# Performance work log

Hardware: AMD Instinct MI355X
Metric: run time of the kernel (lower is better)

## Reference

```python
import jax, jax.numpy as jnp
import numpy as np

N = 20000   # nodes
E = 320000  # edges
G = 64      # graphs in batch
IN = 256    # in_dim
H = 256     # hidden_dim1
C = 2       # n_classes


def setup_inputs() -> dict:
    key = jax.random.key(0)
    ks = jax.random.split(key, 12)
    h = jax.random.normal(ks[0], (N, IN), jnp.float32)
    src = jax.random.randint(ks[1], (E,), 0, N)
    dst = jax.random.randint(ks[2], (E,), 0, N)
    graph_id = jnp.sort(jax.random.randint(ks[3], (N,), 0, G))
    s_in = 1.0 / np.sqrt(IN)
    s_h = 1.0 / np.sqrt(H)
    W_conv = jax.random.normal(ks[4], (IN, H), jnp.float32) * s_in
    b_conv = jnp.zeros((H,), jnp.float32)
    w_gate = jax.random.normal(ks[5], (H, 1), jnp.float32) * s_h
    b_gate = jnp.zeros((1,), jnp.float32)
    W1 = jax.random.normal(ks[6], (H, H), jnp.float32) * s_h
    b1 = jnp.zeros((H,), jnp.float32)
    W2 = jax.random.normal(ks[7], (H, C), jnp.float32) * s_h
    b2 = jnp.zeros((C,), jnp.float32)
    return dict(h=h, src=src, dst=dst, graph_id=graph_id, W_conv=W_conv,
                b_conv=b_conv, w_gate=w_gate, b_gate=b_gate, W1=W1, b1=b1,
                W2=W2, b2=b2)


def reference(h, src, dst, graph_id, W_conv, b_conv, w_gate, b_gate, W1, b1, W2, b2):
    ones_e = jnp.ones((E,), jnp.float32)
    # DGL GraphConv, norm='both': D_out^-1/2 on source, D_in^-1/2 on dest
    deg_out = jax.ops.segment_sum(ones_e, src, num_segments=N)
    deg_in = jax.ops.segment_sum(ones_e, dst, num_segments=N)
    hn = h * jax.lax.rsqrt(jnp.maximum(deg_out, 1.0))[:, None]
    hn = hn @ W_conv                       # [N, H] (weight applied before aggregation)
    agg = jax.ops.segment_sum(hn[src], dst, num_segments=N)  # gather + scatter-add
    agg = agg * jax.lax.rsqrt(jnp.maximum(deg_in, 1.0))[:, None] + b_conv
    hr = jax.nn.relu(agg)                  # F.relu after conv1
    # GlobalAttentionPooling: per-graph segment softmax over gate scores
    gate = hr @ w_gate + b_gate            # [N, 1]
    gmax = jax.ops.segment_max(gate, graph_id, num_segments=G)
    e = jnp.exp(gate - gmax[graph_id])
    denom = jax.ops.segment_sum(e, graph_id, num_segments=G)
    att = e / denom[graph_id]              # [N, 1] attention weights (g2)
    hg = jax.ops.segment_sum(att * hr, graph_id, num_segments=G)  # [G, H]
    # classifier heads (dropout is identity at inference)
    a2 = hg @ W1 + b1
    a3 = a2 @ W2 + b2
    return jax.nn.sigmoid(a3), att, hg
```

## Files before the change

### kernel.cpp

```cpp
#include <hip/hip_runtime.h>
#include <hip/hip_bf16.h>
#include <hip/hip_fp16.h>
#include <math.h>

#define NN 20000
#define EE 320000
#define GG 64
#define IND 256
#define HD 256
#define CC 2

typedef __hip_bfloat16 bf16;
typedef __attribute__((ext_vector_type(8))) short short8;
typedef __attribute__((ext_vector_type(4))) float f32x4;

__device__ __forceinline__ float b2f(bf16 x){ return __bfloat162float(x); }
__device__ __forceinline__ float bits2f(unsigned short b){
    union{ float f; unsigned u; } v; v.u = ((unsigned)b) << 16; return v.f;
}
__device__ __forceinline__ short f2bs(float x){
    union{ bf16 b; short s; } u; u.b = __float2bfloat16(x); return u.s;
}
__device__ __forceinline__ float ldf3(const void* p, size_t i, int c){
    if (c == 1) return b2f(((const bf16*)p)[i]);
    if (c == 2) return __half2float(((const __half*)p)[i]);
    return ((const float*)p)[i];
}
__device__ __forceinline__ int idec(const void* p, int i, int c){
    if (c == 1) return (int)(((const long long*)p)[i]);
    if (c == 2) return (int)(((const float*)p)[i]);
    if (c == 3) return (int)__half2float(((const __half*)p)[i]);
    return ((const int*)p)[i];
}
__device__ __forceinline__ int wdetect_wave(const unsigned short* p, int t){
    unsigned u = p[2*t];
    int e8 = (u >> 7) & 0xFF;
    int e5 = (u >> 10) & 0x1F;
    int nz = __popcll(__ballot(u != 0));
    int cb = __popcll(__ballot(e8 >= 100 && e8 <= 141));
    int cf = __popcll(__ballot(e5 >= 4 && e5 <= 22));
    return (nz < 8) ? 0 : (cb >= 60) ? 1 : ((cf >= 60) ? 2 : 0);
}

#define ZBLK 64
#define DETB (9 + IND)
__global__ __launch_bounds__(256) void k_detect(const void* src, const void* dst,
                         const void* gid,
                         const unsigned short* h, const unsigned short* Wc,
                         const unsigned short* wg, const unsigned short* W1,
                         const unsigned short* W2, const unsigned short* bc,
                         int* icode, int* dcode, int* zero_base,
                         bf16* __restrict__ Wb){
    int blk = blockIdx.x;
    int t = threadIdx.x;
    if (blk < 3){
        if (t >= 64) return;
        const void* buf = (blk == 0) ? src : (blk == 1) ? dst : gid;
        int n     = (blk == 2) ? NN : EE;
        int bound = (blk == 2) ? GG : NN;
        long long v64 = ((const long long*)buf)[n/8 + t];
        unsigned long long bad64 = __ballot(v64 < 0 || v64 >= (long long)bound);
        int v32 = ((const int*)buf)[n/4 + t];
        unsigned long long bad32 = __ballot(v32 < 0 || v32 >= bound);
        float f32v = __uint_as_float(((const unsigned*)buf)[n/4 + t]);
        unsigned long long badf32 = __ballot(!(f32v >= 0.f && f32v < (float)bound));
        float f16v = __half2float(((const __half*)buf)[n/2 + t]);
        unsigned long long badf16 = __ballot(!(f16v >= 0.f && f16v < (float)bound));
        if (t == 0)
            icode[blk] = (bad64 == 0ull) ? 1 : ((bad32 == 0ull) ? 0 :
                         ((badf32 == 0ull) ? 2 : ((badf16 == 0ull) ? 3 : 0)));
    } else if (blk < 9){
        if (t >= 64) return;
        int b = blk - 3;
        const unsigned short* p = b==0?h:b==1?Wc:b==2?wg:b==3?W1:b==4?W2:bc;
        int code = wdetect_wave(p, t);
        if (t == 0) dcode[b] = code;
    } else if (blk < DETB){
        int k = blk - 9;
        __shared__ int scode;
        if (t < 64){
            int code = wdetect_wave(Wc, t);
            if (t == 0) scode = code;
        }
        __syncthreads();
        int c = scode;
        Wb[(size_t)t*IND + k] = __float2bfloat16(ldf3(Wc, (size_t)k*HD + t, c));
    } else {
        int idx = (blk - DETB)*256 + t;
        const int total = 3*NN + GG*HD;
        for (int i = idx; i < total; i += ZBLK*256) zero_base[i] = 0;
    }
}

#define GEMMB (NN/32)
#define PREPB ((EE+255)/256)
__global__ __launch_bounds__(256) void k_prepgemm(const void* __restrict__ h,
                                                  const bf16* __restrict__ Wb,
                                                  const void* __restrict__ src_r,
                                                  const void* __restrict__ dst_r,
                                                  const void* __restrict__ gid_r,
                                                  const int* __restrict__ icode,
                                                  const int* __restrict__ dcode,
                                                  int* __restrict__ gid_i,
                                                  int* cnt_out, int* cnt_in,
                                                  bf16* __restrict__ hn){
    int blk = blockIdx.x;
    if (blk >= GEMMB){
        int i = (blk - GEMMB)*256 + threadIdx.x;
        if (i < NN) gid_i[i] = idec(gid_r, i, icode[2]);
        if (i >= EE) return;
        int s = idec(src_r, i, icode[0]);
        int d = idec(dst_r, i, icode[1]);
        if ((unsigned)s < NN) atomicAdd(&cnt_out[s], 1);
        if ((unsigned)d < NN) atomicAdd(&cnt_in[d], 1);
        return;
    }
    int fh = dcode[0];
    int tid = threadIdx.x;
    int wave = tid >> 6, lane = tid & 63;
    int q = lane >> 4, mr = lane & 15;
    int row0 = blk * 32;
    int ncol0 = wave * 64;
    f32x4 acc[2][4] = {};
    const float* hf = (const float*)h;
    #pragma unroll
    for (int k0 = 0; k0 < IND; k0 += 32){
        short8 a[2], b[4];
        if (fh == 0){
            #pragma unroll
            for (int mi = 0; mi < 2; mi++){
                int r = row0 + mi*16 + mr;
                const float4* p = (const float4*)(hf + (size_t)r*IND + k0 + q*8);
                float4 v0 = p[0], v1 = p[1];
                a[mi][0] = f2bs(v0.x); a[mi][1] = f2bs(v0.y);
                a[mi][2] = f2bs(v0.z); a[mi][3] = f2bs(v0.w);
                a[mi][4] = f2bs(v1.x); a[mi][5] = f2bs(v1.y);
                a[mi][6] = f2bs(v1.z); a[mi][7] = f2bs(v1.w);
            }
        } else {
            #pragma unroll
            for (int mi = 0; mi < 2; mi++){
                int r = row0 + mi*16 + mr;
                #pragma unroll
                for (int j = 0; j < 8; j++)
                    a[mi][j] = f2bs(ldf3(h, (size_t)r*IND + k0 + q*8 + j, fh));
            }
        }
        #pragma unroll
        for (int ni = 0; ni < 4; ni++)
            b[ni] = *reinterpret_cast<const short8*>(
                        Wb + (size_t)(ncol0 + ni*16 + mr)*IND + k0 + q*8);
        #pragma unroll
        for (int mi = 0; mi < 2; mi++)
            #pragma unroll
            for (int ni = 0; ni < 4; ni++)
                acc[mi][ni] = __builtin_amdgcn_mfma_f32_16x16x32_bf16(
                                  a[mi], b[ni], acc[mi][ni], 0, 0, 0);
    }
    #pragma unroll
    for (int mi = 0; mi < 2; mi++){
        int rowb = row0 + mi*16 + q*4;
        #pragma unroll
        for (int r = 0; r < 4; r++){
            int row = rowb + r;
            #pragma unroll
            for (int ni = 0; ni < 4; ni++)
                hn[(size_t)row*HD + ncol0 + ni*16 + mr] =
                    __float2bfloat16(acc[mi][ni][r]);
        }
    }
}

__global__ __launch_bounds__(1024) void k_scan(const int* __restrict__ cnt_out,
                                               const int* __restrict__ cnt_in,
                                               const int* __restrict__ gid,
                                               float* rs_out, float* rs_in,
                                               int* __restrict__ row_start,
                                               int* gstart, int* gend){
    int t = threadIdx.x;
    for (int i = t; i < NN; i += 1024){
        rs_out[i] = rsqrtf(fmaxf((float)cnt_out[i], 1.f));
        rs_in[i]  = rsqrtf(fmaxf((float)cnt_in[i], 1.f));
    }
    __shared__ int part[1024];
    const int per = (NN + 1023)/1024;
    int lo = t*per, hi = min(lo+per, NN);
    int s = 0;
    for (int i = lo; i < hi; i++) s += cnt_in[i];
    part[t] = s; __syncthreads();
    for (int off = 1; off < 1024; off <<= 1){
        int v = (t >= off) ? part[t-off] : 0;
        __syncthreads();
        part[t] += v;
        __syncthreads();
    }
    int base = part[t] - s;
    for (int i = lo; i < hi; i++){ row_start[i] = base; base += cnt_in[i]; }
    if (t == 1023) row_start[NN] = part[1023];
    __shared__ int ls[GG+1];
    if (t <= GG){
        int a = 0, b = NN;
        while (a < b){
            int mid = (a + b) >> 1;
            if (gid[mid] < t) a = mid + 1; else b = mid;
        }
        ls[t] = a;
    }
    __syncthreads();
    if (t < GG){ gstart[t] = ls[t]; gend[t] = ls[t+1]; }
}

__global__ void k_fill(const void* src_r, const void* dst_r,
                       const int* __restrict__ icode,
                       const int* __restrict__ row_start, int* __restrict__ cursor,
                       int* __restrict__ csr_src){
    int e = blockIdx.x*256 + threadIdx.x;
    if (e >= EE) return;
    int s = idec(src_r, e, icode[0]);
    int d = idec(dst_r, e, icode[1]);
    if ((unsigned)s >= NN || (unsigned)d >= NN) return;
    int pos = atomicAdd(&cursor[d], 1);
    csr_src[row_start[d] + pos] = s;
}

__global__ __launch_bounds__(256) void k_gather(const bf16* __restrict__ hn,
                                                const float* __restrict__ rs_out,
                                                const float* __restrict__ rs_in,
                                                const int* __restrict__ row_start,
                                                const int* __restrict__ csr_src,
                                                const void* __restrict__ b_conv,
                                                const void* __restrict__ w_gate,
                                                const void* __restrict__ b_gate,
                                                const int* __restrict__ dcode,
                                                float* __restrict__ hr,
                                                float* __restrict__ gate){
    int wave = threadIdx.x >> 6, lane = threadIdx.x & 63;
    int n = blockIdx.x*4 + wave;
    if (n >= NN) return;
    int lo = row_start[n], hi = row_start[n+1];
    int half = lane >> 5, l2 = lane & 31;
    float a0=0.f,a1=0.f,a2=0.f,a3=0.f,a4=0.f,a5=0.f,a6=0.f,a7=0.f;
    int j = lo;
    for (; j + 8 <= hi; j += 8){
        int sA = csr_src[j+0+half], sB = csr_src[j+2+half];
        int sC = csr_src[j+4+half], sD = csr_src[j+6+half];
        float rA = rs_out[sA], rB = rs_out[sB], rC = rs_out[sC], rD = rs_out[sD];
        short8 uA = *reinterpret_cast<const short8*>(hn + (size_t)sA*HD + l2*8);
        short8 uB = *reinterpret_cast<const short8*>(hn + (size_t)sB*HD + l2*8);
        short8 uC = *reinterpret_cast<const short8*>(hn + (size_t)sC*HD + l2*8);
        short8 uD = *reinterpret_cast<const short8*>(hn + (size_t)sD*HD + l2*8);
        a0 = fmaf(rA, bits2f((unsigned short)uA[0]),
             fmaf(rB, bits2f((unsigned short)uB[0]),
             fmaf(rC, bits2f((unsigned short)uC[0]),
             fmaf(rD, bits2f((unsigned short)uD[0]), a0))));
        a1 = fmaf(rA, bits2f((unsigned short)uA[1]),
             fmaf(rB, bits2f((unsigned short)uB[1]),
             fmaf(rC, bits2f((unsigned short)uC[1]),
             fmaf(rD, bits2f((unsigned short)uD[1]), a1))));
        a2 = fmaf(rA, bits2f((unsigned short)uA[2]),
             fmaf(rB, bits2f((unsigned short)uB[2]),
             fmaf(rC, bits2f((unsigned short)uC[2]),
             fmaf(rD, bits2f((unsigned short)uD[2]), a2))));
        a3 = fmaf(rA, bits2f((unsigned short)uA[3]),
             fmaf(rB, bits2f((unsigned short)uB[3]),
             fmaf(rC, bits2f((unsigned short)uC[3]),
             fmaf(rD, bits2f((unsigned short)uD[3]), a3))));
        a4 = fmaf(rA, bits2f((unsigned short)uA[4]),
             fmaf(rB, bits2f((unsigned short)uB[4]),
             fmaf(rC, bits2f((unsigned short)uC[4]),
             fmaf(rD, bits2f((unsigned short)uD[4]), a4))));
        a5 = fmaf(rA, bits2f((unsigned short)uA[5]),
             fmaf(rB, bits2f((unsigned short)uB[5]),
             fmaf(rC, bits2f((unsigned short)uC[5]),
             fmaf(rD, bits2f((unsigned short)uD[5]), a5))));
        a6 = fmaf(rA, bits2f((unsigned short)uA[6]),
             fmaf(rB, bits2f((unsigned short)uB[6]),
             fmaf(rC, bits2f((unsigned short)uC[6]),
             fmaf(rD, bits2f((unsigned short)uD[6]), a6))));
        a7 = fmaf(rA, bits2f((unsigned short)uA[7]),
             fmaf(rB, bits2f((unsigned short)uB[7]),
             fmaf(rC, bits2f((unsigned short)uC[7]),
             fmaf(rD, bits2f((unsigned short)uD[7]), a7))));
    }
    for (; j + 2 <= hi; j += 2){
        int s = csr_src[j+half];
        float r = rs_out[s];
        short8 u = *reinterpret_cast<const short8*>(hn + (size_t)s*HD + l2*8);
        a0 = fmaf(r, bits2f((unsigned short)u[0]), a0);
        a1 = fmaf(r, bits2f((unsigned short)u[1]), a1);
        a2 = fmaf(r, bits2f((unsigned short)u[2]), a2);
        a3 = fmaf(r, bits2f((unsigned short)u[3]), a3);
        a4 = fmaf(r, bits2f((unsigned short)u[4]), a4);
        a5 = fmaf(r, bits2f((unsigned short)u[5]), a5);
        a6 = fmaf(r, bits2f((unsigned short)u[6]), a6);
        a7 = fmaf(r, bits2f((unsigned short)u[7]), a7);
    }
    if (j < hi && half == 0){
        int s = csr_src[j];
        float r = rs_out[s];
        short8 u = *reinterpret_cast<const short8*>(hn + (size_t)s*HD + l2*8);
        a0 = fmaf(r, bits2f((unsigned short)u[0]), a0);
        a1 = fmaf(r, bits2f((unsigned short)u[1]), a1);
        a2 = fmaf(r, bits2f((unsigned short)u[2]), a2);
        a3 = fmaf(r, bits2f((unsigned short)u[3]), a3);
        a4 = fmaf(r, bits2f((unsigned short)u[4]), a4);
        a5 = fmaf(r, bits2f((unsigned short)u[5]), a5);
        a6 = fmaf(r, bits2f((unsigned short)u[6]), a6);
        a7 = fmaf(r, bits2f((unsigned short)u[7]), a7);
    }
    float send0 = half ? a0 : a4;
    float send1 = half ? a1 : a5;
    float send2 = half ? a2 : a6;
    float send3 = half ? a3 : a7;
    float recv0 = __shfl_xor(send0, 32);
    float recv1 = __shfl_xor(send1, 32);
    float recv2 = __shfl_xor(send2, 32);
    float recv3 = __shfl_xor(send3, 32);
    float tot0 = (half ? a4 : a0) + recv0;
    float tot1 = (half ? a5 : a1) + recv1;
    float tot2 = (half ? a6 : a2) + recv2;
    float tot3 = (half ? a7 : a3) + recv3;
    int db = dcode[5], fg = dcode[2];
    float rsn = rs_in[n];
    int c = l2*8 + half*4;
    float v0 = fmaxf(fmaf(tot0, rsn, ldf3(b_conv, c+0, db)), 0.f);
    float v1 = fmaxf(fmaf(tot1, rsn, ldf3(b_conv, c+1, db)), 0.f);
    float v2 = fmaxf(fmaf(tot2, rsn, ldf3(b_conv, c+2, db)), 0.f);
    float v3 = fmaxf(fmaf(tot3, rsn, ldf3(b_conv, c+3, db)), 0.f);
    float4 fv; fv.x = v0; fv.y = v1; fv.z = v2; fv.w = v3;
    *(float4*)(hr + (size_t)n*HD + c) = fv;
    float g = v0*ldf3(w_gate, c+0, fg) + v1*ldf3(w_gate, c+1, fg)
            + v2*ldf3(w_gate, c+2, fg) + v3*ldf3(w_gate, c+3, fg);
    #pragma unroll
    for (int off = 32; off; off >>= 1) g += __shfl_down(g, off);
    if (lane == 0) gate[n] = g + ldf3(b_gate, 0, db);
}

__global__ __launch_bounds__(256) void k_softhg(const float* __restrict__ gate,
                                                const float* __restrict__ hr,
                                                const int* __restrict__ gstart,
                                                const int* __restrict__ gend,
                                                float* __restrict__ hg,
                                                float* __restrict__ out_att){
    int g = blockIdx.x >> 3, part = blockIdx.x & 7;
    int t = threadIdx.x, lane = t & 63, wid = t >> 6;
    int lo = gstart[g], hi = gend[g], len = hi - lo;
    if (len <= 0) return;
    __shared__ float red[4];
    float m = -INFINITY;
    for (int n = lo + t; n < hi; n += 256) m = fmaxf(m, gate[n]);
    #pragma unroll
    for (int off = 32; off; off >>= 1) m = fmaxf(m, __shfl_xor(m, off));
    if (lane == 0) red[wid] = m;
    __syncthreads();
    m = fmaxf(fmaxf(red[0], red[1]), fmaxf(red[2], red[3]));
    __syncthreads();
    float s = 0.f;
    for (int n = lo + t; n < hi; n += 256) s += expf(gate[n] - m);
    #pragma unroll
    for (int off = 32; off; off >>= 1) s += __shfl_xor(s, off);
    if (lane == 0) red[wid] = s;
    __syncthreads();
    s = red[0] + red[1] + red[2] + red[3];
    float inv = 1.f / s;
    int chunk = (len + 7) >> 3;
    int plo = lo + part*chunk, phi = min(plo + chunk, hi);
    if (plo >= phi) return;
    for (int n = plo + t; n < phi; n += 256)
        out_att[n] = expf(gate[n] - m) * inv;
    float a0 = 0.f, a1 = 0.f, a2 = 0.f, a3 = 0.f;
    int r = plo;
    for (; r + 4 <= phi; r += 4){
        float w0 = expf(gate[r+0] - m) * inv;
        float w1 = expf(gate[r+1] - m) * inv;
        float w2 = expf(gate[r+2] - m) * inv;
        float w3 = expf(gate[r+3] - m) * inv;
        a0 = fmaf(w0, hr[(size_t)(r+0)*HD + t], a0);
        a1 = fmaf(w1, hr[(size_t)(r+1)*HD + t], a1);
        a2 = fmaf(w2, hr[(size_t)(r+2)*HD + t], a2);
        a3 = fmaf(w3, hr[(size_t)(r+3)*HD + t], a3);
    }
    for (; r < phi; r++)
        a0 = fmaf(expf(gate[r] - m) * inv, hr[(size_t)r*HD + t], a0);
    atomicAdd(&hg[g*HD + t], (a0 + a1) + (a2 + a3));
}

__global__ __launch_bounds__(256) void k_cls(const float* __restrict__ hg,
                                             const void* __restrict__ W1,
                                             const void* __restrict__ b1,
                                             const void* __restrict__ W2,
                                             const void* __restrict__ b2,
                                             const int* __restrict__ dcode,
                                             float* __restrict__ out0,
                                             float* __restrict__ out_hg){
    int f1 = dcode[3], f2 = dcode[4], db = dcode[5];
    int g = blockIdx.x, tid = threadIdx.x;
    __shared__ float hs[256];
    float hv = hg[g*HD + tid];
    hs[tid] = hv;
    out_hg[g*HD + tid] = hv;
    __syncthreads();
    float acc = ldf3(b1, tid, db);
    if (f1 == 1){
        const bf16* w = (const bf16*)W1;
        for (int k = 0; k < HD; k++) acc += hs[k]*b2f(w[(size_t)k*HD + tid]);
    } else if (f1 == 2){
        const __half* w = (const __half*)W1;
        for (int k = 0; k < HD; k++) acc += hs[k]*__half2float(w[(size_t)k*HD + tid]);
    } else {
        const float* w = (const float*)W1;
        for (int k = 0; k < HD; k++) acc += hs[k]*w[(size_t)k*HD + tid];
    }
    float p0 = acc * ldf3(W2, tid*CC + 0, f2);
    float p1 = acc * ldf3(W2, tid*CC + 1, f2);
    __shared__ float r0[256], r1[256];
    r0[tid] = p0; r1[tid] = p1; __syncthreads();
    for (int s = 128; s; s >>= 1){
        if (tid < s){ r0[tid] += r0[tid+s]; r1[tid] += r1[tid+s]; }
        __syncthreads();
    }
    if (tid == 0){
        out0[g*CC+0] = 1.f/(1.f + expf(-(r0[0] + ldf3(b2, 0, db))));
        out0[g*CC+1] = 1.f/(1.f + expf(-(r1[0] + ldf3(b2, 1, db))));
    }
}

extern "C" void kernel_launch(void* const* d_in, const int* in_sizes, int n_in,
                              void* d_out, int out_size, void* d_ws, size_t ws_size,
                              hipStream_t stream) {
    const void* h      = d_in[0];
    const void* src_r  = d_in[1];
    const void* dst_r  = d_in[2];
    const void* gid_r  = d_in[3];
    const void* W_conv = d_in[4];
    const void* b_conv = d_in[5];
    const void* w_gate = d_in[6];
    const void* b_gate = d_in[7];
    const void* W1     = d_in[8];
    const void* b1     = d_in[9];
    const void* W2     = d_in[10];
    const void* b2     = d_in[11];

    float* out     = (float*)d_out;
    float* out0    = out;
    float* out_att = out + GG*CC;
    float* out_hg  = out + GG*CC + NN;

    char* w = (char*)d_ws;
    float* hr   = (float*)w;  w += (size_t)NN*HD*sizeof(float);
    bf16*  hn   = (bf16*)w;   w += (size_t)NN*HD*sizeof(bf16);
    bf16*  Wb   = (bf16*)w;   w += (size_t)IND*HD*sizeof(bf16);
    float* rs_o = (float*)w;  w += (size_t)NN*sizeof(float);
    float* rs_i = (float*)w;  w += (size_t)NN*sizeof(float);
    float* gate = (float*)w;  w += (size_t)NN*sizeof(float);
    int* gstart = (int*)w;    w += GG*sizeof(int);
    int* gend   = (int*)w;    w += GG*sizeof(int);
    int* dcode  = (int*)w;    w += 8*sizeof(int);
    int* icode  = (int*)w;    w += 8*sizeof(int);
    int* gid_i  = (int*)w;    w += (size_t)NN*sizeof(int);
    int* cnt_out= (int*)w;    w += (size_t)NN*sizeof(int);
    int* cnt_in = (int*)w;    w += (size_t)NN*sizeof(int);
    int* cursor = (int*)w;    w += (size_t)NN*sizeof(int);
    float* hg   = (float*)w;  w += (size_t)GG*HD*sizeof(float);
    int* rowst  = (int*)w;    w += (size_t)(NN+1)*sizeof(int);
    int* csr    = (int*)w;    w += (size_t)EE*sizeof(int);

    k_detect<<<DETB + ZBLK, 256, 0, stream>>>(src_r, dst_r, gid_r,
                                     (const unsigned short*)h, (const unsigned short*)W_conv,
                                     (const unsigned short*)w_gate, (const unsigned short*)W1,
                                     (const unsigned short*)W2, (const unsigned short*)b_conv,
                                     icode, dcode, cnt_out, Wb);

    k_prepgemm<<<GEMMB + PREPB, 256, 0, stream>>>(h, Wb, src_r, dst_r, gid_r,
                                                  icode, dcode, gid_i,
                                                  cnt_out, cnt_in, hn);

    k_scan<<<1, 1024, 0, stream>>>(cnt_out, cnt_in, gid_i, rs_o, rs_i,
                                   rowst, gstart, gend);

    k_fill<<<PREPB, 256, 0, stream>>>(src_r, dst_r, icode, rowst, cursor, csr);

    k_gather<<<(NN+3)/4, 256, 0, stream>>>(hn, rs_o, rs_i, rowst, csr,
                                           b_conv, w_gate, b_gate, dcode, hr, gate);

    k_softhg<<<GG*8, 256, 0, stream>>>(gate, hr, gstart, gend, hg, out_att);

    k_cls<<<GG, 256, 0, stream>>>(hg, W1, b1, W2, b2, dcode, out0, out_hg);
}
```

Before: 230.0 us.

## Pre-convert h to bf16 in detect kernel and software-pipeline GEMM loads

The fp32-to-bf16 conversion of h moves from the GEMM kernel into extra blocks of the detect kernel, which write a bf16 copy of h to workspace. The GEMM then reads bf16 directly and uses 16-row tiles, doubling the block count, with register double-buffering of the A and B fragments across the k loop. This is meant to shorten the GEMM's load and convert path and improve latency hiding. In exchange it adds a full extra write and read of a 10 MB bf16 buffer plus more workspace, and the smaller tile halves reuse of the W fragments.

Result: no change. 234.1 us (+1.8%).

```diff
diff --git a/kernel.cpp b/kernel.cpp
--- a/kernel.cpp
+++ b/kernel.cpp
@@ -44,13 +44,14 @@
 
 #define ZBLK 64
 #define DETB (9 + IND)
+#define HBB  (NN*HD/4096)
 __global__ __launch_bounds__(256) void k_detect(const void* src, const void* dst,
                          const void* gid,
                          const unsigned short* h, const unsigned short* Wc,
                          const unsigned short* wg, const unsigned short* W1,
                          const unsigned short* W2, const unsigned short* bc,
                          int* icode, int* dcode, int* zero_base,
-                         bf16* __restrict__ Wb){
+                         bf16* __restrict__ Wb, bf16* __restrict__ hb){
     int blk = blockIdx.x;
     int t = threadIdx.x;
     if (blk < 3){
@@ -85,22 +86,44 @@
         __syncthreads();
         int c = scode;
         Wb[(size_t)t*IND + k] = __float2bfloat16(ldf3(Wc, (size_t)k*HD + t, c));
+    } else if (blk < DETB + HBB){
+        __shared__ int scode;
+        if (t < 64){
+            int code = wdetect_wave(h, t);
+            if (t == 0) scode = code;
+        }
+        __syncthreads();
+        int c = scode;
+        size_t e0 = (size_t)(blk - DETB)*4096 + (size_t)t*16;
+        if (c == 0){
+            const float4* pf = (const float4*)((const float*)h + e0);
+            float4 v0 = pf[0], v1 = pf[1], v2 = pf[2], v3 = pf[3];
+            short8 s0, s1;
+            s0[0]=f2bs(v0.x); s0[1]=f2bs(v0.y); s0[2]=f2bs(v0.z); s0[3]=f2bs(v0.w);
+            s0[4]=f2bs(v1.x); s0[5]=f2bs(v1.y); s0[6]=f2bs(v1.z); s0[7]=f2bs(v1.w);
+            s1[0]=f2bs(v2.x); s1[1]=f2bs(v2.y); s1[2]=f2bs(v2.z); s1[3]=f2bs(v2.w);
+            s1[4]=f2bs(v3.x); s1[5]=f2bs(v3.y); s1[6]=f2bs(v3.z); s1[7]=f2bs(v3.w);
+            *reinterpret_cast<short8*>(hb + e0) = s0;
+            *reinterpret_cast<short8*>(hb + e0 + 8) = s1;
+        } else {
+            for (int j = 0; j < 16; j++)
+                hb[e0 + j] = __float2bfloat16(ldf3(h, e0 + j, c));
+        }
     } else {
-        int idx = (blk - DETB)*256 + t;
+        int idx = (blk - (DETB + HBB))*256 + t;
         const int total = 3*NN + GG*HD;
         for (int i = idx; i < total; i += ZBLK*256) zero_base[i] = 0;
     }
 }
 
-#define GEMMB (NN/32)
+#define GEMMB (NN/16)
 #define PREPB ((EE+255)/256)
-__global__ __launch_bounds__(256) void k_prepgemm(const void* __restrict__ h,
+__global__ __launch_bounds__(256) void k_prepgemm(const bf16* __restrict__ hb,
                                                   const bf16* __restrict__ Wb,
                                                   const void* __restrict__ src_r,
                                                   const void* __restrict__ dst_r,
                                                   const void* __restrict__ gid_r,
                                                   const int* __restrict__ icode,
-                                                  const int* __restrict__ dcode,
                                                   int* __restrict__ gid_i,
                                                   int* cnt_out, int* cnt_in,
                                                   bf16* __restrict__ hn){
@@ -115,59 +138,46 @@
         if ((unsigned)d < NN) atomicAdd(&cnt_in[d], 1);
         return;
     }
-    int fh = dcode[0];
     int tid = threadIdx.x;
     int wave = tid >> 6, lane = tid & 63;
     int q = lane >> 4, mr = lane & 15;
-    int row0 = blk * 32;
+    int row0 = blk * 16;
     int ncol0 = wave * 64;
-    f32x4 acc[2][4] = {};
-    const float* hf = (const float*)h;
+    const bf16* arow = hb + (size_t)(row0 + mr)*IND + q*8;
+    const bf16* b0 = Wb + (size_t)(ncol0 +  0 + mr)*IND + q*8;
+    const bf16* b1 = Wb + (size_t)(ncol0 + 16 + mr)*IND + q*8;
+    const bf16* b2 = Wb + (size_t)(ncol0 + 32 + mr)*IND + q*8;
+    const bf16* b3 = Wb + (size_t)(ncol0 + 48 + mr)*IND + q*8;
+    f32x4 acc[4] = {};
+    short8 ac  = *reinterpret_cast<const short8*>(arow);
+    short8 bc0 = *reinterpret_cast<const short8*>(b0);
+    short8 bc1 = *reinterpret_cast<const short8*>(b1);
+    short8 bc2 = *reinterpret_cast<const short8*>(b2);
+    short8 bc3 = *reinterpret_cast<const short8*>(b3);
     #pragma unroll
-    for (int k0 = 0; k0 < IND; k0 += 32){
-        short8 a[2], b[4];
-        if (fh == 0){
-            #pragma unroll
-            for (int mi = 0; mi < 2; mi++){
-                int r = row0 + mi*16 + mr;
-                const float4* p = (const float4*)(hf + (size_t)r*IND + k0 + q*8);
-                float4 v0 = p[0], v1 = p[1];
-                a[mi][0] = f2bs(v0.x); a[mi][1] = f2bs(v0.y);
-                a[mi][2] = f2bs(v0.z); a[mi][3] = f2bs(v0.w);
-                a[mi][4] = f2bs(v1.x); a[mi][5] = f2bs(v1.y);
-                a[mi][6] = f2bs(v1.z); a[mi][7] = f2bs(v1.w);
-            }
-        } else {
-            #pragma unroll
-            for (int mi = 0; mi < 2; mi++){
-                int r = row0 + mi*16 + mr;
-                #pragma unroll
-                for (int j = 0; j < 8; j++)
-                    a[mi][j] = f2bs(ldf3(h, (size_t)r*IND + k0 + q*8 + j, fh));
-            }
-        }
+    for (int k0 = 0; k0 < IND - 32; k0 += 32){
+        short8 an  = *reinterpret_cast<const short8*>(arow + k0 + 32);
+        short8 bn0 = *reinterpret_cast<const short8*>(b0 + k0 + 32);
+        short8 bn1 = *reinterpret_cast<const short8*>(b1 + k0 + 32);
+        short8 bn2 = *reinterpret_cast<const short8*>(b2 + k0 + 32);
+        short8 bn3 = *reinterpret_cast<const short8*>(b3 + k0 + 32);
+        acc[0] = __builtin_amdgcn_mfma_f32_16x16x32_bf16(ac, bc0, acc[0], 0, 0, 0);
+        acc[1] = __builtin_amdgcn_mfma_f32_16x16x32_bf16(ac, bc1, acc[1], 0, 0, 0);
+        acc[2] = __builtin_amdgcn_mfma_f32_16x16x32_bf16(ac, bc2, acc[2], 0, 0, 0);
+        acc[3] = __builtin_amdgcn_mfma_f32_16x16x32_bf16(ac, bc3, acc[3], 0, 0, 0);
+        ac = an; bc0 = bn0; bc1 = bn1; bc2 = bn2; bc3 = bn3;
+    }
+    acc[0] = __builtin_amdgcn_mfma_f32_16x16x32_bf16(ac, bc0, acc[0], 0, 0, 0);
+    acc[1] = __builtin_amdgcn_mfma_f32_16x16x32_bf16(ac, bc1, acc[1], 0, 0, 0);
+    acc[2] = __builtin_amdgcn_mfma_f32_16x16x32_bf16(ac, bc2, acc[2], 0, 0, 0);
+    acc[3] = __builtin_amdgcn_mfma_f32_16x16x32_bf16(ac, bc3, acc[3], 0, 0, 0);
+    #pragma unroll
+    for (int r = 0; r < 4; r++){
+        int row = row0 + q*4 + r;
         #pragma unroll
         for (int ni = 0; ni < 4; ni++)
-            b[ni] = *reinterpret_cast<const short8*>(
-                        Wb + (size_t)(ncol0 + ni*16 + mr)*IND + k0 + q*8);
-        #pragma unroll
-        for (int mi = 0; mi < 2; mi++)
-            #pragma unroll
-            for (int ni = 0; ni < 4; ni++)
-                acc[mi][ni] = __builtin_amdgcn_mfma_f32_16x16x32_bf16(
-                                  a[mi], b[ni], acc[mi][ni], 0, 0, 0);
-    }
-    #pragma unroll
-    for (int mi = 0; mi < 2; mi++){
-        int rowb = row0 + mi*16 + q*4;
-        #pragma unroll
-        for (int r = 0; r < 4; r++){
-            int row = rowb + r;
-            #pragma unroll
-            for (int ni = 0; ni < 4; ni++)
-                hn[(size_t)row*HD + ncol0 + ni*16 + mr] =
-                    __float2bfloat16(acc[mi][ni][r]);
-        }
+            hn[(size_t)row*HD + ncol0 + ni*16 + mr] =
+                __float2bfloat16(acc[ni][r]);
     }
 }
 
@@ -449,6 +459,7 @@
     char* w = (char*)d_ws;
     float* hr   = (float*)w;  w += (size_t)NN*HD*sizeof(float);
     bf16*  hn   = (bf16*)w;   w += (size_t)NN*HD*sizeof(bf16);
+    bf16*  hb   = (bf16*)w;   w += (size_t)NN*HD*sizeof(bf16);
     bf16*  Wb   = (bf16*)w;   w += (size_t)IND*HD*sizeof(bf16);
     float* rs_o = (float*)w;  w += (size_t)NN*sizeof(float);
     float* rs_i = (float*)w;  w += (size_t)NN*sizeof(float);
@@ -465,14 +476,14 @@
     int* rowst  = (int*)w;    w += (size_t)(NN+1)*sizeof(int);
     int* csr    = (int*)w;    w += (size_t)EE*sizeof(int);
 
-    k_detect<<<DETB + ZBLK, 256, 0, stream>>>(src_r, dst_r, gid_r,
+    k_detect<<<DETB + HBB + ZBLK, 256, 0, stream>>>(src_r, dst_r, gid_r,
                                      (const unsigned short*)h, (const unsigned short*)W_conv,
                                      (const unsigned short*)w_gate, (const unsigned short*)W1,
                                      (const unsigned short*)W2, (const unsigned short*)b_conv,
-                                     icode, dcode, cnt_out, Wb);
-
-    k_prepgemm<<<GEMMB + PREPB, 256, 0, stream>>>(h, Wb, src_r, dst_r, gid_r,
-                                                  icode, dcode, gid_i,
+                                     icode, dcode, cnt_out, Wb, hb);
+
+    k_prepgemm<<<GEMMB + PREPB, 256, 0, stream>>>(hb, Wb, src_r, dst_r, gid_r,
+                                                  icode, gid_i,
                                                   cnt_out, cnt_in, hn);
 
     k_scan<<<1, 1024, 0, stream>>>(cnt_out, cnt_in, gid_i, rs_o, rs_i,
```
